# Performance work log

Measured on AMD Instinct MI355X. Metric: run time of the kernel, lower is better.

## Reference

```python
import jax, jax.numpy as jnp
import numpy as np

N = 50000      # nodes
E = 800000     # edges (avg degree 16)
DIN = 256      # input_dim
DH = 128       # hidden_dim
ALPHA_LOGIT = 0.6190392084062235  # logit(0.65)


def setup_inputs() -> dict:
    key = jax.random.key(0)
    ks = jax.random.split(key, 12)
    f = lambda k, s: jax.random.normal(k, s, dtype=jnp.float32)
    return {
        "x": f(ks[0], (N, DIN)),
        "edge_index": jax.random.randint(ks[1], (2, E), 0, N, dtype=jnp.int32),
        "reranker_scores": f(ks[2], (N,)),
        # input_proj
        "Wp": f(ks[3], (DIN, DH)) * 0.02, "bp": jnp.zeros((DH,), jnp.float32),
        # SAGEConv 0: lin_l (aggregated neighbors, with bias), lin_r (root, no bias)
        "Wl0": f(ks[4], (DIN, DH)) * 0.02, "bl0": jnp.zeros((DH,), jnp.float32),
        "Wr0": f(ks[5], (DIN, DH)) * 0.02,
        # SAGEConv 1
        "Wl1": f(ks[6], (DH, DH)) * 0.02, "bl1": jnp.zeros((DH,), jnp.float32),
        "Wr1": f(ks[7], (DH, DH)) * 0.02,
        # score head MLP
        "W1": f(ks[8], (DH, DH // 2)) * 0.02, "b1": jnp.zeros((DH // 2,), jnp.float32),
        "W2": f(ks[9], (DH // 2, 1)) * 0.02, "b2": jnp.zeros((1,), jnp.float32),
        "alpha_logit": jnp.float32(ALPHA_LOGIT),
    }


def _sage_conv(h, src, dst, Wl, bl, Wr):
    # PyG SAGEConv (aggr='mean', root_weight=True):
    # out = lin_l(mean_{j in N(i)} h_j) + lin_r(h_i)
    msg = h[src]                                             # [E, d] gather
    agg = jax.ops.segment_sum(msg, dst, num_segments=N)      # [N, d]
    cnt = jax.ops.segment_sum(jnp.ones((src.shape[0],), h.dtype), dst, num_segments=N)
    agg = agg / jnp.maximum(cnt, 1.0)[:, None]               # mean; isolated nodes -> 0
    return agg @ Wl + bl + h @ Wr


def reference(x, edge_index, reranker_scores, Wp, bp, Wl0, bl0, Wr0,
              Wl1, bl1, Wr1, W1, b1, W2, b2, alpha_logit):
    src, dst = edge_index[0], edge_index[1]
    # norm_type='none' -> no input normalization; eval mode -> dropout is identity
    residual = x @ Wp + bp                                   # [N, DH]
    h = jax.nn.relu(_sage_conv(x, src, dst, Wl0, bl0, Wr0)) + residual
    h = jax.nn.relu(_sage_conv(h, src, dst, Wl1, bl1, Wr1)) + h
    gnn_scores = (jax.nn.relu(h @ W1 + b1) @ W2 + b2)[:, 0]  # [N]
    alpha = jax.nn.sigmoid(alpha_logit)
    return alpha * reranker_scores + (1.0 - alpha) * gnn_scores
```

## Files before the change

kernel.cpp:

```cpp
#include <hip/hip_runtime.h>
#include <hip/hip_bf16.h>


#define DIN 256
#define DH 128
#define NPB 256
#define LOG_NPB 8
#define NBMAX 256
#define EPB 2048
#define JL (EPB/256)
#define SLOTS 8192

typedef __attribute__((ext_vector_type(8))) short short8;
typedef __attribute__((ext_vector_type(4))) float float4v;
typedef __attribute__((ext_vector_type(2))) float float2v;

__device__ inline ushort f2b(float f){
  unsigned u = __float_as_uint(f);
  u = (u + 0x7fffu + ((u >> 16) & 1u)) >> 16;
  return (ushort)u;
}
__device__ inline float blo(unsigned v){ return __uint_as_float(v << 16); }
__device__ inline float bhi(unsigned v){ return __uint_as_float(v & 0xffff0000u); }
__device__ inline short8 pack8(float4 f0, float4 f1){
  short8 v;
  v[0]=(short)f2b(f0.x); v[1]=(short)f2b(f0.y); v[2]=(short)f2b(f0.z); v[3]=(short)f2b(f0.w);
  v[4]=(short)f2b(f1.x); v[5]=(short)f2b(f1.y); v[6]=(short)f2b(f1.z); v[7]=(short)f2b(f1.w);
  return v;
}
__device__ inline void glds16(const ushort* g, ushort* l){
  __builtin_amdgcn_global_load_lds((const __attribute__((address_space(1))) void*)g,
                                   (__attribute__((address_space(3))) void*)l, 16, 0, 0);
}
__device__ inline unsigned char enc8(float v){
  return (unsigned char)(__builtin_amdgcn_cvt_pk_fp8_f32(v, v, 0, false) & 0xFF);
}
__device__ inline float2v dec8(unsigned u){
  return __builtin_amdgcn_cvt_pk_f32_fp8((int)u, false);
}

__device__ inline void gather16x2(const ushort* __restrict__ a8,
    const ushort* __restrict__ adj, int pA, int eA, int pB, int eB, int lane,
    float2v& aA, float2v& aB)
{
  while (pA < eA || pB < eB){
    ushort uA[16], uB[16];
    bool dA = pA < eA, dB = pB < eB;
    if (dA){
      #pragma unroll
      for (int j=0;j<16;j++){
        int ix = __builtin_amdgcn_readfirstlane((int)adj[pA+j]);
        uA[j] = a8[(size_t)ix*64 + lane];
      }
    }
    if (dB){
      #pragma unroll
      for (int j=0;j<16;j++){
        int ix = __builtin_amdgcn_readfirstlane((int)adj[pB+j]);
        uB[j] = a8[(size_t)ix*64 + lane];
      }
    }
    if (dA){
      #pragma unroll
      for (int j=0;j<16;j++) aA += dec8(uA[j]);
      pA += 16;
    }
    if (dB){
      #pragma unroll
      for (int j=0;j<16;j++) aB += dec8(uB[j]);
      pB += 16;
    }
  }
}

__global__ __launch_bounds__(256) void fused_front(
    const float* __restrict__ x, int N, ushort* __restrict__ xb, int nstripe,
    const float* __restrict__ Wp, const float* __restrict__ Wl0, const float* __restrict__ Wr0,
    const float* __restrict__ Wl1, const float* __restrict__ Wr1, const float* __restrict__ W1,
    ushort* __restrict__ Wpf, ushort* __restrict__ Wl0f, ushort* __restrict__ Wr0f,
    ushort* __restrict__ Wl1f, ushort* __restrict__ Wr1f, ushort* __restrict__ W1f,
    const int* __restrict__ src, const int* __restrict__ dst, int E, int NB,
    int* __restrict__ bucketCnt, int* __restrict__ pairS, int* __restrict__ pairD,
    int nPart, int nConv)
{
  __shared__ int hist[NBMAX], lbase[NBMAX], gbase[NBMAX], lcur[NBMAX], sc[NBMAX];
  __shared__ int ls[EPB], ld[EPB];
  int bid = blockIdx.x;
  int t = threadIdx.x;

  if (bid < nPart){
    int base = bid * EPB;
    int cntE = E - base; if (cntE > EPB) cntE = EPB;
    for (int i=t;i<NB;i+=256) hist[i]=0;
    __syncthreads();
    int myS[JL], myD[JL];
    #pragma unroll
    for (int j=0;j<JL;j++){
      int e = base + j*256 + t;
      if (e < E){ myS[j]=src[e]; myD[j]=dst[e]; atomicAdd(&hist[myD[j]>>LOG_NPB],1); }
      else myD[j] = -1;
    }
    __syncthreads();
    if (t < NBMAX) sc[t] = (t < NB)? hist[t] : 0;
    __syncthreads();
    for (int st=1; st<NBMAX; st<<=1){
      int v = 0;
      if (t < NBMAX && t >= st) v = sc[t-st];
      __syncthreads();
      if (t < NBMAX) sc[t] += v;
      __syncthreads();
    }
    if (t < NB){
      int excl = (t>0)? sc[t-1] : 0;
      lbase[t] = excl; lcur[t] = excl;
      gbase[t] = atomicAdd(&bucketCnt[t], hist[t]);
    }
    __syncthreads();
    #pragma unroll
    for (int j=0;j<JL;j++){
      if (myD[j] >= 0){
        int b = myD[j] >> LOG_NPB;
        int p = atomicAdd(&lcur[b], 1);
        ls[p] = myS[j]; ld[p] = myD[j];
      }
    }
    __syncthreads();
    for (int i=t;i<cntE;i+=256){
      int d = ld[i];
      int b = d >> LOG_NPB;
      int p = gbase[b] + (i - lbase[b]);
      if (p < SLOTS){
        pairS[(size_t)b*SLOTS + p] = ls[i];
        pairD[(size_t)b*SLOTS + p] = d;
      }
    }
  } else if (bid < nPart + nConv){
    int gi = (bid - nPart)*256 + t;
    if (gi < nstripe*512){
      int L = gi & 63, ks = (gi>>6)&7, s = gi>>9;
      int row = s*16 + (L&15);
      int k = ks*32 + (L>>4)*8;
      short8 v;
      if (row < N){
        const float* p = x + (size_t)row*DIN + k;
        v = pack8(*(const float4*)p, *(const float4*)(p+4));
      } else {
        #pragma unroll
        for (int j=0;j<8;j++) v[j]=0;
      }
      *(short8*)(xb + (size_t)gi*8) = v;
    }
  } else {
    int gi = (bid - nPart - nConv)*256 + t;
    if (gi < 17408){
      const float* sw; ushort* dw; int cols, b0;
      if      (gi <  4096){ sw=Wp;  dw=Wpf;  cols=128; b0=0; }
      else if (gi <  8192){ sw=Wl0; dw=Wl0f; cols=128; b0=4096; }
      else if (gi < 12288){ sw=Wr0; dw=Wr0f; cols=128; b0=8192; }
      else if (gi < 14336){ sw=Wl1; dw=Wl1f; cols=128; b0=12288; }
      else if (gi < 16384){ sw=Wr1; dw=Wr1f; cols=128; b0=14336; }
      else                { sw=W1;  dw=W1f;  cols=64;  b0=16384; }
      int i = gi - b0;
      int ln = i & 63, g = i >> 6;
      int ntq = cols >> 4;
      int nt = g % ntq, ks = g / ntq;
      int col = nt*16 + (ln & 15);
      int k0 = ks*32 + (ln >> 4)*8;
      short8 v;
      #pragma unroll
      for (int j=0;j<8;j++) v[j] = (short)f2b(sw[(size_t)(k0+j)*cols + col]);
      *(short8*)(dw + (size_t)i*8) = v;
    }
  }
}

__global__ __launch_bounds__(256) void gemm0_csr(
    const ushort* __restrict__ xb, int N, int nstripe, int ngemm, int nbuck,
    const ushort* __restrict__ Wpf, const ushort* __restrict__ Wl0f, const ushort* __restrict__ Wr0f,
    const float* __restrict__ bp,
    ushort* __restrict__ xp, unsigned char* __restrict__ q8, ushort* __restrict__ xr0,
    const int* __restrict__ bucketCnt, const int* __restrict__ pairS, const int* __restrict__ pairD,
    int* __restrict__ off, int* __restrict__ deg, ushort* __restrict__ adj)
{
  __shared__ __align__(16) ushort smem[32768];
  int bid = blockIdx.x, t = threadIdx.x;

  if (bid >= nbuck){
    int g = bid - nbuck;
    int xcd = g & 7, jj = g >> 3;
    int mat = jj % 3;
    int b = xcd + 8*(jj/3);
    int nblk = ngemm / 3;
    const ushort* Wf = (mat==0)? Wpf : (mat==1)? Wl0f : Wr0f;
    int w = t>>6, lane = t&63, lq = lane&15, quad = lane>>4;
    #pragma unroll
    for (int j=0;j<16;j++){
      int gg = w + j*4;
      glds16(Wf + (size_t)gg*512 + lane*8, smem + gg*512);
    }
    __syncthreads();
    float bias[8];
    #pragma unroll
    for (int nt=0;nt<8;nt++) bias[nt] = (mat==0)? bp[nt*16 + lq] : 0.f;
    int nchunk = (nstripe + 3) >> 2;

#define LOADAV(AV, cc) do { \
    int stripe_ = (cc)*4 + w; \
    if (stripe_ < nstripe){ \
      _Pragma("unroll") \
      for (int ks=0;ks<8;ks++) \
        AV[ks] = *(const short8*)(xb + ((size_t)stripe_*8 + ks)*512 + lane*8); \
    } \
  } while(0)

#define COMPSTORE(AV, cc) do { \
    int stripe_ = (cc)*4 + w; \
    if (stripe_ < nstripe){ \
      int row0_ = stripe_*16; \
      float4v acc_[8]; \
      _Pragma("unroll") for (int nt=0;nt<8;nt++){ \
        _Pragma("unroll") for (int r=0;r<4;r++) acc_[nt][r]=0.f; } \
      _Pragma("unroll") for (int ks=0;ks<8;ks++){ \
        _Pragma("unroll") for (int nt=0;nt<8;nt++){ \
          short8 bf_ = *(const short8*)(smem + (size_t)((ks*8+nt)*64 + lane)*8); \
          acc_[nt] = __builtin_amdgcn_mfma_f32_16x16x32_bf16(AV[ks], bf_, acc_[nt], 0,0,0); \
        } \
      } \
      if (mat == 1){ \
        _Pragma("unroll") for (int nt=0;nt<8;nt++) \
        _Pragma("unroll") for (int r=0;r<4;r++){ \
          int row_ = row0_ + quad*4 + r; \
          if (row_ < N) q8[(size_t)row_*128 + nt*16 + lq] = enc8(acc_[nt][r]); \
        } \
      } else { \
        ushort* Y_ = (mat==0)? xp : xr0; \
        _Pragma("unroll") for (int nt=0;nt<8;nt++) \
        _Pragma("unroll") for (int r=0;r<4;r++){ \
          int row_ = row0_ + quad*4 + r; \
          if (row_ < N) Y_[(size_t)row_*128 + nt*16 + lq] = f2b(acc_[nt][r] + bias[nt]); \
        } \
      } \
    } \
  } while(0)

    short8 avA[8], avB[8];
    int c = b;
    if (c < nchunk){
      LOADAV(avA, c);
      while (true){
        int cn = c + nblk;
        if (cn < nchunk) LOADAV(avB, cn);
        COMPSTORE(avA, c);
        c = cn;
        if (c >= nchunk) break;
        cn = c + nblk;
        if (cn < nchunk) LOADAV(avA, cn);
        COMPSTORE(avB, c);
        c = cn;
        if (c >= nchunk) break;
      }
    }
#undef LOADAV
#undef COMPSTORE
  } else {
    int b = bid;
    int* cnt  = (int*)smem;
    int* offl = cnt + 256;
    int* s1   = offl + 257;
    ushort* win = (ushort*)(s1 + 256);
    int node0 = b * NPB;
    int base  = b * SLOTS;
    int ce = bucketCnt[b]; if (ce > SLOTS) ce = SLOTS;
    int ce4 = ce & ~3;
    cnt[t] = 0;
    __syncthreads();
    for (int i = t*4; i < ce4; i += 1024){
      int4 dd = *(const int4*)(pairD + base + i);
      atomicAdd(&cnt[dd.x - node0], 1);
      atomicAdd(&cnt[dd.y - node0], 1);
      atomicAdd(&cnt[dd.z - node0], 1);
      atomicAdd(&cnt[dd.w - node0], 1);
    }
    for (int i = ce4 + t; i < ce; i += 256)
      atomicAdd(&cnt[pairD[(size_t)base+i] - node0], 1);
    __syncthreads();
    int a = cnt[t];
    int pa = (a + 15) & ~15;
    s1[t] = pa;
    __syncthreads();
    for (int st=1; st<256; st<<=1){
      int v = (t>=st)? s1[t-st] : 0;
      __syncthreads();
      s1[t] += v;
      __syncthreads();
    }
    int excl = (t>0)? s1[t-1] : 0;
    offl[t] = excl;
    int ptotal = s1[255]; if (ptotal > SLOTS) ptotal = SLOTS;
    int node = node0 + t;
    if (node < N){ off[node] = base + excl; deg[node] = a; }
    __syncthreads();
    for (int i=t;i<ptotal;i+=256) win[i] = (ushort)N;
    __syncthreads();
    for (int i = t*4; i < ce4; i += 1024){
      int4 dd = *(const int4*)(pairD + base + i);
      int4 ss = *(const int4*)(pairS + base + i);
      int p0 = atomicAdd(&offl[dd.x - node0], 1); if (p0 < SLOTS) win[p0] = (ushort)ss.x;
      int p1 = atomicAdd(&offl[dd.y - node0], 1); if (p1 < SLOTS) win[p1] = (ushort)ss.y;
      int p2 = atomicAdd(&offl[dd.z - node0], 1); if (p2 < SLOTS) win[p2] = (ushort)ss.z;
      int p3 = atomicAdd(&offl[dd.w - node0], 1); if (p3 < SLOTS) win[p3] = (ushort)ss.w;
    }
    for (int i = ce4 + t; i < ce; i += 256){
      int dd = pairD[(size_t)base+i];
      int p = atomicAdd(&offl[dd - node0], 1);
      if (p < SLOTS) win[p] = (ushort)pairS[(size_t)base+i];
    }
    __syncthreads();
    for (int i=t;i<ptotal;i+=256) adj[(size_t)base+i] = win[i];
  }
}

__global__ __launch_bounds__(256) void combine0_f8(
    const unsigned char* __restrict__ agg8, const ushort* __restrict__ rootsrc,
    const ushort* __restrict__ ressrc, const float* __restrict__ bias,
    const int* __restrict__ off, const int* __restrict__ deg,
    const ushort* __restrict__ adj, ushort* __restrict__ out, int n)
{
  int t = threadIdx.x;
  int d = t & 63, w = t >> 6;
  int nA = blockIdx.x*8 + w*2, nB = nA + 1;
  if (nA >= n) return;
  const ushort* a8 = (const ushort*)agg8;
  bool vB = nB < n;
  unsigned rtA = ((const unsigned*)rootsrc)[(size_t)nA*64 + d];
  unsigned rsA = ((const unsigned*)ressrc)[(size_t)nA*64 + d];
  unsigned rtB = 0, rsB = 0;
  int pA = off[nA], cA = deg[nA], eA = pA + ((cA + 15) & ~15);
  int pB = 0, cB = 0, eB = 0;
  if (vB){
    rtB = ((const unsigned*)rootsrc)[(size_t)nB*64 + d];
    rsB = ((const unsigned*)ressrc)[(size_t)nB*64 + d];
    pB = off[nB]; cB = deg[nB]; eB = pB + ((cB + 15) & ~15);
  }
  float2v aA = {0.f, 0.f}, aB = {0.f, 0.f};
  gather16x2(a8, adj, pA, eA, pB, eB, d, aA, aB);
  float b0 = bias[2*d], b1v = bias[2*d+1];
  float invA = 1.f / (float)((cA > 1)? cA : 1);
  float o0 = fmaxf(aA[0]*invA + b0  + blo(rtA), 0.f) + blo(rsA);
  float o1 = fmaxf(aA[1]*invA + b1v + bhi(rtA), 0.f) + bhi(rsA);
  ((unsigned*)out)[(size_t)nA*64 + d] = (unsigned)f2b(o0) | ((unsigned)f2b(o1) << 16);
  if (vB){
    float invB = 1.f / (float)((cB > 1)? cB : 1);
    float q0 = fmaxf(aB[0]*invB + b0  + blo(rtB), 0.f) + blo(rsB);
    float q1 = fmaxf(aB[1]*invB + b1v + bhi(rtB), 0.f) + bhi(rsB);
    ((unsigned*)out)[(size_t)nB*64 + d] = (unsigned)f2b(q0) | ((unsigned)f2b(q1) << 16);
  }
}

__global__ __launch_bounds__(256) void gemm1_wres(
    const ushort* __restrict__ h, int N,
    const ushort* __restrict__ Wl1f, const ushort* __restrict__ Wr1f,
    unsigned char* __restrict__ q8, ushort* __restrict__ hr1)
{
  __shared__ __align__(16) ushort Bs[32768];
  int t = threadIdx.x, w = t>>6, lane = t&63, lq = lane&15, quad = lane>>4;
  int tile = blockIdx.x;
  #pragma unroll
  for (int j=0;j<16;j++){
    int r = w + j*4;
    int m = r>>5, g = r&31;
    const ushort* Wm = m ? Wr1f : Wl1f;
    glds16(Wm + (size_t)g*512 + lane*8, Bs + r*512);
  }
  short8 av[2][4];
  int row0 = tile*128 + w*32;
  #pragma unroll
  for (int mt=0;mt<2;mt++){
    int row = row0 + mt*16 + lq; if (row >= N) row = N-1;
    #pragma unroll
    for (int ks=0;ks<4;ks++)
      av[mt][ks] = *(const short8*)(h + (size_t)row*128 + ks*32 + quad*8);
  }
  __syncthreads();
  #pragma unroll
  for (int m=0;m<2;m++){
    float4v acc[2][8];
    #pragma unroll
    for (int i=0;i<2;i++)
      #pragma unroll
      for (int j=0;j<8;j++)
        #pragma unroll
        for (int r=0;r<4;r++) acc[i][j][r] = 0.f;
    #pragma unroll
    for (int ks=0;ks<4;ks++){
      #pragma unroll
      for (int nt=0;nt<8;nt++){
        short8 bf = *(const short8*)(Bs + ((m*32 + ks*8 + nt)*64 + lane)*8);
        acc[0][nt] = __builtin_amdgcn_mfma_f32_16x16x32_bf16(av[0][ks], bf, acc[0][nt], 0,0,0);
        acc[1][nt] = __builtin_amdgcn_mfma_f32_16x16x32_bf16(av[1][ks], bf, acc[1][nt], 0,0,0);
      }
    }
    #pragma unroll
    for (int mt=0;mt<2;mt++){
      #pragma unroll
      for (int r=0;r<4;r++){
        int row = row0 + mt*16 + quad*4 + r;
        if (row < N){
          if (m == 0){
            #pragma unroll
            for (int nt=0;nt<8;nt++)
              q8[(size_t)row*128 + nt*16 + lq] = enc8(acc[mt][nt][r]);
          } else {
            #pragma unroll
            for (int nt=0;nt<8;nt++)
              hr1[(size_t)row*128 + nt*16 + lq] = f2b(acc[mt][nt][r]);
          }
        }
      }
    }
  }
}

__global__ __launch_bounds__(256) void head_mlp(
    const ushort* __restrict__ h2, int n,
    const ushort* __restrict__ W1f, const float* __restrict__ b1,
    const float* __restrict__ W2, const float* __restrict__ b2,
    const float* __restrict__ alogit, const float* __restrict__ rer,
    float* __restrict__ out)
{
  __shared__ __align__(16) ushort W1s[8192];
  int t = threadIdx.x, w = t>>6, lane = t&63, lq = lane&15, quad = lane>>4;
  #pragma unroll
  for (int j=0;j<4;j++){
    int g = w + j*4;
    glds16(W1f + (size_t)g*512 + lane*8, W1s + g*512);
  }
  int row0 = blockIdx.x*128 + w*32;
  short8 av[2][4];
  #pragma unroll
  for (int mt=0;mt<2;mt++){
    int row = row0 + mt*16 + lq; if (row >= n) row = n-1;
    #pragma unroll
    for (int ks=0;ks<4;ks++)
      av[mt][ks] = *(const short8*)(h2 + (size_t)row*128 + ks*32 + quad*8);
  }
  __syncthreads();
  float4v acc[2][4];
  #pragma unroll
  for (int mt=0;mt<2;mt++)
    #pragma unroll
    for (int nt=0;nt<4;nt++)
      #pragma unroll
      for (int r=0;r<4;r++) acc[mt][nt][r] = 0.f;
  #pragma unroll
  for (int ks=0;ks<4;ks++){
    #pragma unroll
    for (int nt=0;nt<4;nt++){
      short8 bf = *(const short8*)(W1s + ((ks*4 + nt)*64 + lane)*8);
      acc[0][nt] = __builtin_amdgcn_mfma_f32_16x16x32_bf16(av[0][ks], bf, acc[0][nt], 0,0,0);
      acc[1][nt] = __builtin_amdgcn_mfma_f32_16x16x32_bf16(av[1][ks], bf, acc[1][nt], 0,0,0);
    }
  }
  float al = alogit[0];
  float a  = 1.f / (1.f + __expf(-al));
  #pragma unroll
  for (int mt=0;mt<2;mt++){
    float pw[4] = {0.f,0.f,0.f,0.f};
    #pragma unroll
    for (int nt=0; nt<4; nt++){
      int c = nt*16 + lq;
      float w2 = W2[c];
      float bb = b1[c];
      #pragma unroll
      for (int r=0; r<4; r++)
        pw[r] += fmaxf(acc[mt][nt][r] + bb, 0.f) * w2;
    }
    #pragma unroll
    for (int mask=1; mask<16; mask<<=1){
      #pragma unroll
      for (int r=0; r<4; r++)
        pw[r] += __shfl_xor(pw[r], mask);
    }
    if (lq == 0){
      #pragma unroll
      for (int r=0; r<4; r++){
        int row = row0 + mt*16 + quad*4 + r;
        if (row < n)
          out[row] = a * rer[row] + (1.f - a) * (pw[r] + b2[0]);
      }
    }
  }
}

extern "C" void kernel_launch(void* const* d_in, const int* in_sizes, int n_in,
                              void* d_out, int out_size, void* d_ws, size_t ws_size,
                              hipStream_t stream)
{
  (void)n_in; (void)out_size; (void)ws_size;
  const float* x    = (const float*)d_in[0];
  const int*   ei   = (const int*)d_in[1];
  const float* rer  = (const float*)d_in[2];
  const float* Wp   = (const float*)d_in[3];
  const float* bp   = (const float*)d_in[4];
  const float* Wl0  = (const float*)d_in[5];
  const float* bl0  = (const float*)d_in[6];
  const float* Wr0  = (const float*)d_in[7];
  const float* Wl1  = (const float*)d_in[8];
  const float* bl1  = (const float*)d_in[9];
  const float* Wr1  = (const float*)d_in[10];
  const float* W1   = (const float*)d_in[11];
  const float* b1   = (const float*)d_in[12];
  const float* W2   = (const float*)d_in[13];
  const float* b2   = (const float*)d_in[14];
  const float* alogit = (const float*)d_in[15];

  const int N = in_sizes[2];
  const int E = in_sizes[1] / 2;
  const int* src = ei;
  const int* dst = ei + E;
  const int NB = (N + NPB - 1) / NPB;
  const int nstripe = (N + 15) / 16;
  const int ntile = (N + 127) / 128;
  const int nPart = (E + EPB - 1) / EPB;
  const int nConv = (nstripe*512 + 255)/256;

  ushort* U = (ushort*)d_ws;
  ushort* xb  = U;
  ushort* xp  = xb + (size_t)nstripe*512*8;
  ushort* xr0 = xp  + (size_t)N*DH;
  ushort* h   = xr0 + (size_t)N*DH;
  unsigned char* q8 = (unsigned char*)(h + (size_t)N*DH);
  ushort* Wpf  = (ushort*)(q8 + (size_t)(N+1)*DH);
  ushort* Wl0f = Wpf  + (size_t)4096*8;
  ushort* Wr0f = Wl0f + (size_t)4096*8;
  ushort* Wl1f = Wr0f + (size_t)4096*8;
  ushort* Wr1f = Wl1f + (size_t)2048*8;
  ushort* W1f  = Wr1f + (size_t)2048*8;
  int* I = (int*)(W1f + (size_t)1024*8);
  int* bucketCnt = I;
  int* off   = bucketCnt + NBMAX;
  int* deg   = off + N;
  int* pairS = deg + N;
  int* pairD = pairS + (size_t)NB*SLOTS;
  ushort* adj = (ushort*)(pairD + (size_t)NB*SLOTS);
  ushort* h2  = xb;

  hipMemsetAsync(bucketCnt, 0, NBMAX*sizeof(int), stream);
  hipMemsetAsync(q8 + (size_t)N*DH, 0, DH, stream);

  fused_front<<<nPart + nConv + 68, 256, 0, stream>>>(
      x, N, xb, nstripe, Wp, Wl0, Wr0, Wl1, Wr1, W1,
      Wpf, Wl0f, Wr0f, Wl1f, Wr1f, W1f,
      src, dst, E, NB, bucketCnt, pairS, pairD, nPart, nConv);

  gemm0_csr<<<NB + 768, 256, 0, stream>>>(
      xb, N, nstripe, 768, NB, Wpf, Wl0f, Wr0f, bp, xp, q8, xr0,
      bucketCnt, pairS, pairD, off, deg, adj);

  combine0_f8<<<(N+7)/8, 256, 0, stream>>>(q8, xr0, xp, bl0, off, deg, adj, h, N);

  gemm1_wres<<<ntile, 256, 0, stream>>>(h, N, Wl1f, Wr1f, q8, xr0);

  combine0_f8<<<(N+7)/8, 256, 0, stream>>>(q8, xr0, h, bl1, off, deg, adj, h2, N);

  head_mlp<<<ntile, 256, 0, stream>>>(h2, N, W1f, b1, W2, b2, alogit, rer, (float*)d_out);
}
```

Before: 218.3 us.

## Split fp8 aggregation table into column halves and double combine grid

The fp8 projected-neighbor table is stored as two separate 64-column arrays, and the combine kernel launches twice as many blocks, each handling one half of the feature dimension. Each gather then touches 64-byte rows, halving the random-access working set per block, which is meant to improve L2/MALL locality. In exchange, adjacency lists and degrees are read twice, and per-lane loads become single bytes with narrower stores.

After: 252.2 us. 15.5% more time.

```diff
diff --git a/kernel.cpp b/kernel.cpp
--- a/kernel.cpp
+++ b/kernel.cpp
@@ -22,6 +22,7 @@
 }
 __device__ inline float blo(unsigned v){ return __uint_as_float(v << 16); }
 __device__ inline float bhi(unsigned v){ return __uint_as_float(v & 0xffff0000u); }
+__device__ inline float b2f(ushort v){ return __uint_as_float(((unsigned)v) << 16); }
 __device__ inline short8 pack8(float4 f0, float4 f1){
   short8 v;
   v[0]=(short)f2b(f0.x); v[1]=(short)f2b(f0.y); v[2]=(short)f2b(f0.z); v[3]=(short)f2b(f0.w);
@@ -39,12 +40,12 @@
   return __builtin_amdgcn_cvt_pk_f32_fp8((int)u, false);
 }
 
-__device__ inline void gather16x2(const ushort* __restrict__ a8,
+__device__ inline void gather16x2b(const unsigned char* __restrict__ a8,
     const ushort* __restrict__ adj, int pA, int eA, int pB, int eB, int lane,
-    float2v& aA, float2v& aB)
+    float& aA, float& aB)
 {
   while (pA < eA || pB < eB){
-    ushort uA[16], uB[16];
+    unsigned char uA[16], uB[16];
     bool dA = pA < eA, dB = pB < eB;
     if (dA){
       #pragma unroll
@@ -62,12 +63,20 @@
     }
     if (dA){
       #pragma unroll
-      for (int j=0;j<16;j++) aA += dec8(uA[j]);
+      for (int j=0;j<8;j++){
+        unsigned u = (unsigned)uA[2*j] | ((unsigned)uA[2*j+1] << 8);
+        float2v f = dec8(u);
+        aA += f[0] + f[1];
+      }
       pA += 16;
     }
     if (dB){
       #pragma unroll
-      for (int j=0;j<16;j++) aB += dec8(uB[j]);
+      for (int j=0;j<8;j++){
+        unsigned u = (unsigned)uB[2*j] | ((unsigned)uB[2*j+1] << 8);
+        float2v f = dec8(u);
+        aB += f[0] + f[1];
+      }
       pB += 16;
     }
   }
@@ -178,7 +187,8 @@
     const ushort* __restrict__ xb, int N, int nstripe, int ngemm, int nbuck,
     const ushort* __restrict__ Wpf, const ushort* __restrict__ Wl0f, const ushort* __restrict__ Wr0f,
     const float* __restrict__ bp,
-    ushort* __restrict__ xp, unsigned char* __restrict__ q8, ushort* __restrict__ xr0,
+    ushort* __restrict__ xp, unsigned char* __restrict__ q8lo, unsigned char* __restrict__ q8hi,
+    ushort* __restrict__ xr0,
     const int* __restrict__ bucketCnt, const int* __restrict__ pairS, const int* __restrict__ pairD,
     int* __restrict__ off, int* __restrict__ deg, ushort* __restrict__ adj)
 {
@@ -230,7 +240,10 @@
         _Pragma("unroll") for (int nt=0;nt<8;nt++) \
         _Pragma("unroll") for (int r=0;r<4;r++){ \
           int row_ = row0_ + quad*4 + r; \
-          if (row_ < N) q8[(size_t)row_*128 + nt*16 + lq] = enc8(acc_[nt][r]); \
+          if (row_ < N){ \
+            if (nt < 4) q8lo[(size_t)row_*64 + nt*16 + lq] = enc8(acc_[nt][r]); \
+            else        q8hi[(size_t)row_*64 + (nt-4)*16 + lq] = enc8(acc_[nt][r]); \
+          } \
         } \
       } else { \
         ushort* Y_ = (mat==0)? xp : xr0; \
@@ -320,47 +333,50 @@
   }
 }
 
-__global__ __launch_bounds__(256) void combine0_f8(
-    const unsigned char* __restrict__ agg8, const ushort* __restrict__ rootsrc,
-    const ushort* __restrict__ ressrc, const float* __restrict__ bias,
+__global__ __launch_bounds__(256) void combine_f8h(
+    const unsigned char* __restrict__ q8lo, const unsigned char* __restrict__ q8hi,
+    const ushort* __restrict__ rootsrc, const ushort* __restrict__ ressrc,
+    const float* __restrict__ bias,
     const int* __restrict__ off, const int* __restrict__ deg,
-    const ushort* __restrict__ adj, ushort* __restrict__ out, int n)
+    const ushort* __restrict__ adj, ushort* __restrict__ out, int n, int nbh)
 {
   int t = threadIdx.x;
   int d = t & 63, w = t >> 6;
-  int nA = blockIdx.x*8 + w*2, nB = nA + 1;
+  int b = blockIdx.x;
+  int half = (b >= nbh) ? 1 : 0;
+  int nA = (b - half*nbh)*8 + w*2, nB = nA + 1;
   if (nA >= n) return;
-  const ushort* a8 = (const ushort*)agg8;
+  const unsigned char* a8 = half ? q8hi : q8lo;
+  int hd = half*64 + d;
   bool vB = nB < n;
-  unsigned rtA = ((const unsigned*)rootsrc)[(size_t)nA*64 + d];
-  unsigned rsA = ((const unsigned*)ressrc)[(size_t)nA*64 + d];
-  unsigned rtB = 0, rsB = 0;
+  ushort rtA = rootsrc[(size_t)nA*128 + hd];
+  ushort rsA = ressrc[(size_t)nA*128 + hd];
+  ushort rtB = 0, rsB = 0;
   int pA = off[nA], cA = deg[nA], eA = pA + ((cA + 15) & ~15);
   int pB = 0, cB = 0, eB = 0;
   if (vB){
-    rtB = ((const unsigned*)rootsrc)[(size_t)nB*64 + d];
-    rsB = ((const unsigned*)ressrc)[(size_t)nB*64 + d];
+    rtB = rootsrc[(size_t)nB*128 + hd];
+    rsB = ressrc[(size_t)nB*128 + hd];
     pB = off[nB]; cB = deg[nB]; eB = pB + ((cB + 15) & ~15);
   }
-  float2v aA = {0.f, 0.f}, aB = {0.f, 0.f};
-  gather16x2(a8, adj, pA, eA, pB, eB, d, aA, aB);
-  float b0 = bias[2*d], b1v = bias[2*d+1];
+  float aA = 0.f, aB = 0.f;
+  gather16x2b(a8, adj, pA, eA, pB, eB, d, aA, aB);
+  float bv = bias[hd];
   float invA = 1.f / (float)((cA > 1)? cA : 1);
-  float o0 = fmaxf(aA[0]*invA + b0  + blo(rtA), 0.f) + blo(rsA);
-  float o1 = fmaxf(aA[1]*invA + b1v + bhi(rtA), 0.f) + bhi(rsA);
-  ((unsigned*)out)[(size_t)nA*64 + d] = (unsigned)f2b(o0) | ((unsigned)f2b(o1) << 16);
+  float o0 = fmaxf(aA*invA + bv + b2f(rtA), 0.f) + b2f(rsA);
+  out[(size_t)nA*128 + hd] = f2b(o0);
   if (vB){
     float invB = 1.f / (float)((cB > 1)? cB : 1);
-    float q0 = fmaxf(aB[0]*invB + b0  + blo(rtB), 0.f) + blo(rsB);
-    float q1 = fmaxf(aB[1]*invB + b1v + bhi(rtB), 0.f) + bhi(rsB);
-    ((unsigned*)out)[(size_t)nB*64 + d] = (unsigned)f2b(q0) | ((unsigned)f2b(q1) << 16);
+    float o1 = fmaxf(aB*invB + bv + b2f(rtB), 0.f) + b2f(rsB);
+    out[(size_t)nB*128 + hd] = f2b(o1);
   }
 }
 
 __global__ __launch_bounds__(256) void gemm1_wres(
     const ushort* __restrict__ h, int N,
     const ushort* __restrict__ Wl1f, const ushort* __restrict__ Wr1f,
-    unsigned char* __restrict__ q8, ushort* __restrict__ hr1)
+    unsigned char* __restrict__ q8lo, unsigned char* __restrict__ q8hi,
+    ushort* __restrict__ hr1)
 {
   __shared__ __align__(16) ushort Bs[32768];
   int t = threadIdx.x, w = t>>6, lane = t&63, lq = lane&15, quad = lane>>4;
@@ -408,8 +424,10 @@
         if (row < N){
           if (m == 0){
             #pragma unroll
-            for (int nt=0;nt<8;nt++)
-              q8[(size_t)row*128 + nt*16 + lq] = enc8(acc[mt][nt][r]);
+            for (int nt=0;nt<8;nt++){
+              if (nt < 4) q8lo[(size_t)row*64 + nt*16 + lq] = enc8(acc[mt][nt][r]);
+              else        q8hi[(size_t)row*64 + (nt-4)*16 + lq] = enc8(acc[mt][nt][r]);
+            }
           } else {
             #pragma unroll
             for (int nt=0;nt<8;nt++)
@@ -523,14 +541,16 @@
   const int ntile = (N + 127) / 128;
   const int nPart = (E + EPB - 1) / EPB;
   const int nConv = (nstripe*512 + 255)/256;
+  const int nbh = (N + 7) / 8;
 
   ushort* U = (ushort*)d_ws;
   ushort* xb  = U;
   ushort* xp  = xb + (size_t)nstripe*512*8;
   ushort* xr0 = xp  + (size_t)N*DH;
   ushort* h   = xr0 + (size_t)N*DH;
-  unsigned char* q8 = (unsigned char*)(h + (size_t)N*DH);
-  ushort* Wpf  = (ushort*)(q8 + (size_t)(N+1)*DH);
+  unsigned char* q8lo = (unsigned char*)(h + (size_t)N*DH);
+  unsigned char* q8hi = q8lo + (size_t)(N+1)*64;
+  ushort* Wpf  = (ushort*)(q8hi + (size_t)(N+1)*64);
   ushort* Wl0f = Wpf  + (size_t)4096*8;
   ushort* Wr0f = Wl0f + (size_t)4096*8;
   ushort* Wl1f = Wr0f + (size_t)4096*8;
@@ -546,7 +566,8 @@
   ushort* h2  = xb;
 
   hipMemsetAsync(bucketCnt, 0, NBMAX*sizeof(int), stream);
-  hipMemsetAsync(q8 + (size_t)N*DH, 0, DH, stream);
+  hipMemsetAsync(q8lo + (size_t)N*64, 0, 64, stream);
+  hipMemsetAsync(q8hi + (size_t)N*64, 0, 64, stream);
 
   fused_front<<<nPart + nConv + 68, 256, 0, stream>>>(
       x, N, xb, nstripe, Wp, Wl0, Wr0, Wl1, Wr1, W1,
@@ -554,14 +575,14 @@
       src, dst, E, NB, bucketCnt, pairS, pairD, nPart, nConv);
 
   gemm0_csr<<<NB + 768, 256, 0, stream>>>(
-      xb, N, nstripe, 768, NB, Wpf, Wl0f, Wr0f, bp, xp, q8, xr0,
+      xb, N, nstripe, 768, NB, Wpf, Wl0f, Wr0f, bp, xp, q8lo, q8hi, xr0,
       bucketCnt, pairS, pairD, off, deg, adj);
 
-  combine0_f8<<<(N+7)/8, 256, 0, stream>>>(q8, xr0, xp, bl0, off, deg, adj, h, N);
-
-  gemm1_wres<<<ntile, 256, 0, stream>>>(h, N, Wl1f, Wr1f, q8, xr0);
-
-  combine0_f8<<<(N+7)/8, 256, 0, stream>>>(q8, xr0, h, bl1, off, deg, adj, h2, N);
+  combine_f8h<<<2*nbh, 256, 0, stream>>>(q8lo, q8hi, xr0, xp, bl0, off, deg, adj, h, N, nbh);
+
+  gemm1_wres<<<ntile, 256, 0, stream>>>(h, N, Wl1f, Wr1f, q8lo, q8hi, xr0);
+
+  combine_f8h<<<2*nbh, 256, 0, stream>>>(q8lo, q8hi, xr0, h, bl1, off, deg, adj, h2, N, nbh);
 
   head_mlp<<<ntile, 256, 0, stream>>>(h2, N, W1f, b1, W2, b2, alogit, rer, (float*)d_out);
 }
```
